# Kernel optimization log

Hardware: AMD Instinct MI355X
Metric: run time of the kernel (lower is better)

Reference implementation:

```python
import jax, jax.numpy as jnp
import numpy as np

B, N = 262144, 64
CLIP_RATIO = 0.2
DUAL_CLIP = 5.0
USE_VALUE_CLIP = True
HALF_LOG_2PI = 0.5 * float(np.log(2.0 * np.pi))


def setup_inputs() -> dict:
    key = jax.random.key(0)
    ks = jax.random.split(key, 9)
    return {
        "mu_new": jax.random.normal(ks[0], (B, N), jnp.float32),
        "sigma_new": jax.random.uniform(ks[1], (B, N), jnp.float32, 0.5, 1.5),
        "mu_old": jax.random.normal(ks[2], (B, N), jnp.float32),
        "sigma_old": jax.random.uniform(ks[3], (B, N), jnp.float32, 0.5, 1.5),
        "action": jax.random.normal(ks[4], (B, N), jnp.float32),
        "value_new": jax.random.normal(ks[5], (B,), jnp.float32),
        "value_old": jax.random.normal(ks[6], (B,), jnp.float32),
        "adv": jax.random.normal(ks[7], (B,), jnp.float32),
        "return_": jax.random.normal(ks[8], (B,), jnp.float32),
        "weight": jnp.ones((B,), jnp.float32),
    }


def _gauss_logprob(action, mu, sigma):
    # independent Normal log-prob, summed over action dim -> (B,)
    z = (action - mu) / sigma
    return jnp.sum(-0.5 * z * z - jnp.log(sigma) - HALF_LOG_2PI, axis=-1)


def reference(mu_new, sigma_new, mu_old, sigma_old, action,
              value_new, value_old, adv, return_, weight):
    logp_new = _gauss_logprob(action, mu_new, sigma_new)   # (B,)
    logp_old = _gauss_logprob(action, mu_old, sigma_old)   # (B,) constant w.r.t. new params
    ratio = jnp.exp(logp_new - logp_old)

    surr1 = ratio * adv
    surr2 = jnp.clip(ratio, 1.0 - CLIP_RATIO, 1.0 + CLIP_RATIO) * adv
    clipped = jnp.minimum(surr1, surr2)
    # dual clip (arXiv:1912.09729 Eq. 5)
    clipped = jnp.maximum(clipped, DUAL_CLIP * adv)
    policy_loss = -jnp.mean(clipped * weight)

    # entropy of diagonal Gaussian, summed over N
    entropy = jnp.sum(0.5 + HALF_LOG_2PI + jnp.log(sigma_new), axis=-1)
    entropy_loss = jnp.mean(entropy * weight)

    if USE_VALUE_CLIP:
        value_clip = value_old + jnp.clip(value_new - value_old, -CLIP_RATIO, CLIP_RATIO)
        v1 = jnp.square(return_ - value_new)
        v2 = jnp.square(return_ - value_clip)
        value_loss = 0.5 * jnp.mean(jnp.maximum(v1, v2) * weight)
    else:
        value_loss = 0.5 * jnp.mean(jnp.square(return_ - value_new) * weight)

    approx_kl = jnp.mean(logp_old - logp_new)
    clipfrac = jnp.mean((jnp.abs(ratio - 1.0) > CLIP_RATIO).astype(jnp.float32))
    return policy_loss, value_loss, entropy_loss, approx_kl, clipfrac
```

## Files before the change

kernel.cpp:

```cpp
#include <hip/hip_runtime.h>

static constexpr int   N_DIM        = 64;
static constexpr float HALF_LOG_2PI = 0.9189385332046727f;
static constexpr float CLIP_RATIO   = 0.2f;
static constexpr float DUAL_CLIP    = 5.0f;
static constexpr int   GRID         = 2048;
static constexpr float ENT_CONST    = (float)N_DIM * (0.5f + HALF_LOG_2PI);
static constexpr float ENT_C16      = ENT_CONST / 16.0f;

__device__ __forceinline__ void ppo_set(const float4& mn, const float4& sn,
                                        const float4& mo, const float4& so,
                                        const float4& a,
                                        float& en_out, float& d_out)
{
    float qn = 0.f, qo = 0.f;
    float pn = 1.f, po = 1.f;
#define PPO_COMP(c) {                                        \
        float rn = __builtin_amdgcn_rcpf(sn.c);              \
        float zn = (a.c - mn.c) * rn;  qn += zn * zn;        \
        float ro = __builtin_amdgcn_rcpf(so.c);              \
        float zo = (a.c - mo.c) * ro;  qo += zo * zo;        \
        pn *= sn.c;  po *= so.c; }
    PPO_COMP(x) PPO_COMP(y) PPO_COMP(z) PPO_COMP(w)
#undef PPO_COMP
    const float en = __logf(pn);
    const float eo = __logf(po);
    en_out = en;
    d_out  = 0.5f * (qo - qn) + (eo - en);
}

__device__ __forceinline__ void ppo_tail(float en, float d, float w, float ad,
                                         float& accP, float& accE,
                                         float& accK, float& accC)
{
    accK -= d;
    accE += w * (en + ENT_C16);
#pragma unroll
    for (int m = 1; m < 16; m <<= 1) d += __shfl_xor(d, m, 16);
    const float ratio = __expf(d);
    const float rc = fminf(fmaxf(ratio, 1.f - CLIP_RATIO), 1.f + CLIP_RATIO);
    float cl = fminf(ratio * ad, rc * ad);
    cl = fmaxf(cl, DUAL_CLIP * ad);
    accP += cl * w;
    accC += (fabsf(ratio - 1.f) > CLIP_RATIO) ? 1.f : 0.f;
}

__global__ __launch_bounds__(256, 4) void ppo_main(
    const float* __restrict__ mu_new,
    const float* __restrict__ sg_new,
    const float* __restrict__ mu_old,
    const float* __restrict__ sg_old,
    const float* __restrict__ act,
    const float* __restrict__ vnew,
    const float* __restrict__ vold,
    const float* __restrict__ adv,
    const float* __restrict__ ret,
    const float* __restrict__ wgt,
    float* __restrict__ ws,
    int b_rows)
{
    const int t    = threadIdx.x;
    const int wave = t >> 6;
    const int lane = t & 63;
    const int sub  = lane >> 4;

    float accP = 0.f, accV = 0.f, accE = 0.f, accK = 0.f, accC = 0.f;

    {
        const int r = blockIdx.x * 256 + t;
        if (r < b_rows) {
            const float vn = vnew[r], vo = vold[r], rt = ret[r], w = wgt[r];
            const float vc = vo + fminf(fmaxf(vn - vo, -CLIP_RATIO), CLIP_RATIO);
            const float d1 = rt - vn, d2 = rt - vc;
            accV += fmaxf(d1 * d1, d2 * d2) * w;
        }
    }

    const int n_sets = b_rows >> 2;
    const int stride = gridDim.x << 2;
    const int lofs   = lane * 4;
    int s = (blockIdx.x << 2) + wave;

#define PPO_LOAD(P) {                                            \
        const int off = (s << 8) + lofs;                         \
        const int r   = (s << 2) + sub;                          \
        P##mn = *(const float4*)(mu_new + off);                  \
        P##sn = *(const float4*)(sg_new + off);                  \
        P##mo = *(const float4*)(mu_old + off);                  \
        P##so = *(const float4*)(sg_old + off);                  \
        P##a  = *(const float4*)(act    + off);                  \
        P##w  = wgt[r];  P##ad = adv[r];                         \
        s += stride; }

#define PPO_COMPUTE(P) {                                         \
        float en, d;                                             \
        ppo_set(P##mn, P##sn, P##mo, P##so, P##a, en, d);        \
        ppo_tail(en, d, P##w, P##ad, accP, accE, accK, accC); }

    if (s < n_sets) {
        float4 Amn, Asn, Amo, Aso, Aa;  float Aw, Aad;
        float4 Bmn, Bsn, Bmo, Bso, Ba;  float Bw, Bad;

        PPO_LOAD(A);
        bool pendA = true;
        while (s < n_sets) {
            PPO_LOAD(B);
            PPO_COMPUTE(A);
            pendA = false;
            if (s < n_sets) { PPO_LOAD(A); pendA = true; }
            PPO_COMPUTE(B);
        }
        if (pendA) PPO_COMPUTE(A);
    }
#undef PPO_LOAD
#undef PPO_COMPUTE

    accP *= 0.0625f;
    accC *= 0.0625f;

#pragma unroll
    for (int m = 1; m < 64; m <<= 1) {
        accP += __shfl_xor(accP, m, 64);
        accV += __shfl_xor(accV, m, 64);
        accE += __shfl_xor(accE, m, 64);
        accK += __shfl_xor(accK, m, 64);
        accC += __shfl_xor(accC, m, 64);
    }

    __shared__ float red[4][5];
    if (lane == 0) {
        red[wave][0] = accP; red[wave][1] = accV; red[wave][2] = accE;
        red[wave][3] = accK; red[wave][4] = accC;
    }
    __syncthreads();

    if (t == 0) {
        float sm[5] = {0.f, 0.f, 0.f, 0.f, 0.f};
#pragma unroll
        for (int wv = 0; wv < 4; ++wv)
#pragma unroll
            for (int k = 0; k < 5; ++k) sm[k] += red[wv][k];
#pragma unroll
        for (int k = 0; k < 5; ++k) ws[k * GRID + blockIdx.x] = sm[k];
    }
}

__global__ __launch_bounds__(320) void ppo_reduce(
    const float* __restrict__ ws, float* __restrict__ out, int b_rows)
{
    const int wave = threadIdx.x >> 6;
    const int lane = threadIdx.x & 63;

    float v = 0.f;
    for (int i = lane; i < GRID; i += 64) v += ws[wave * GRID + i];
#pragma unroll
    for (int m = 1; m < 64; m <<= 1) v += __shfl_xor(v, m, 64);

    if (lane == 0) {
        const float invB = 1.0f / (float)b_rows;
        float o;
        if      (wave == 0) o = -v * invB;
        else if (wave == 1) o = 0.5f * v * invB;
        else                o = v * invB;
        out[wave] = o;
    }
}

extern "C" void kernel_launch(void* const* d_in, const int* in_sizes, int n_in,
                              void* d_out, int out_size, void* d_ws, size_t ws_size,
                              hipStream_t stream) {
    const float* mu_new = (const float*)d_in[0];
    const float* sg_new = (const float*)d_in[1];
    const float* mu_old = (const float*)d_in[2];
    const float* sg_old = (const float*)d_in[3];
    const float* act    = (const float*)d_in[4];
    const float* vnew   = (const float*)d_in[5];
    const float* vold   = (const float*)d_in[6];
    const float* adv    = (const float*)d_in[7];
    const float* ret    = (const float*)d_in[8];
    const float* wgt    = (const float*)d_in[9];
    float* out = (float*)d_out;
    float* ws  = (float*)d_ws;

    const int b_rows = in_sizes[5];

    ppo_main<<<GRID, 256, 0, stream>>>(mu_new, sg_new, mu_old, sg_old, act,
                                       vnew, vold, adv, ret, wgt,
                                       ws, b_rows);
    ppo_reduce<<<1, 320, 0, stream>>>(ws, out, b_rows);
}
```

Measured before the change: 316.0 us.

## Stream row tiles into double-buffered LDS via async global_load_lds

Replaces the direct float4 register loads of the five (B,64) input streams with asynchronous global-to-LDS copies (global_load_lds, 16 bytes per lane) into a per-wave double-buffered shared-memory tile. Explicit s_waitcnt vmcnt waits gate each compute step, and the block reduction scratch is moved into a corner of the same LDS buffer. The aim is to cut vector register pressure from prefetched data and keep more loads in flight on this bandwidth-bound kernel. In exchange it uses about 40KB of LDS per block, which may limit occupancy, and adds LDS read traffic plus hand-managed wait counts.

```diff
diff --git a/kernel.cpp b/kernel.cpp
--- a/kernel.cpp
+++ b/kernel.cpp
@@ -7,6 +7,14 @@
 static constexpr int   GRID         = 2048;
 static constexpr float ENT_CONST    = (float)N_DIM * (0.5f + HALF_LOG_2PI);
 static constexpr float ENT_C16      = ENT_CONST / 16.0f;
+
+__device__ __forceinline__ void async_cp16(const float* g, float* l)
+{
+    __builtin_amdgcn_global_load_lds(
+        (const __attribute__((address_space(1))) void*)g,
+        (__attribute__((address_space(3))) void*)l,
+        16, 0, 0);
+}
 
 __device__ __forceinline__ void ppo_set(const float4& mn, const float4& sn,
                                         const float4& mo, const float4& so,
@@ -59,6 +67,8 @@
     float* __restrict__ ws,
     int b_rows)
 {
+    __shared__ __align__(16) float lds[4][2][5][256];
+
     const int t    = threadIdx.x;
     const int wave = t >> 6;
     const int lane = t & 63;
@@ -78,41 +88,57 @@
 
     const int n_sets = b_rows >> 2;
     const int stride = gridDim.x << 2;
-    const int lofs   = lane * 4;
+    const int lofs   = lane << 2;
     int s = (blockIdx.x << 2) + wave;
 
-#define PPO_LOAD(P) {                                            \
-        const int off = (s << 8) + lofs;                         \
+#define PPO_ISSUE(BUF, P) {                                      \
         const int r   = (s << 2) + sub;                          \
-        P##mn = *(const float4*)(mu_new + off);                  \
-        P##sn = *(const float4*)(sg_new + off);                  \
-        P##mo = *(const float4*)(mu_old + off);                  \
-        P##so = *(const float4*)(sg_old + off);                  \
-        P##a  = *(const float4*)(act    + off);                  \
         P##w  = wgt[r];  P##ad = adv[r];                         \
+        float* lp = &lds[wave][BUF][0][0];                       \
+        const int gof = (s << 8) + lofs;                         \
+        async_cp16(mu_new + gof, lp + 0 * 256);                  \
+        async_cp16(sg_new + gof, lp + 1 * 256);                  \
+        async_cp16(mu_old + gof, lp + 2 * 256);                  \
+        async_cp16(sg_old + gof, lp + 3 * 256);                  \
+        async_cp16(act    + gof, lp + 4 * 256);                  \
         s += stride; }
 
-#define PPO_COMPUTE(P) {                                         \
+#define PPO_WAIT(N) do {                                          \
+        asm volatile("s_waitcnt vmcnt(" #N ")" ::: "memory");     \
+        __builtin_amdgcn_sched_barrier(0); } while (0)
+
+#define PPO_COMPUTE(BUF, P) {                                    \
+        const float* lp = &lds[wave][BUF][0][0];                 \
+        const float4 mn = *(const float4*)(lp + 0 * 256 + lofs); \
+        const float4 sn = *(const float4*)(lp + 1 * 256 + lofs); \
+        const float4 mo = *(const float4*)(lp + 2 * 256 + lofs); \
+        const float4 so = *(const float4*)(lp + 3 * 256 + lofs); \
+        const float4 a  = *(const float4*)(lp + 4 * 256 + lofs); \
         float en, d;                                             \
-        ppo_set(P##mn, P##sn, P##mo, P##so, P##a, en, d);        \
+        ppo_set(mn, sn, mo, so, a, en, d);                       \
         ppo_tail(en, d, P##w, P##ad, accP, accE, accK, accC); }
 
     if (s < n_sets) {
-        float4 Amn, Asn, Amo, Aso, Aa;  float Aw, Aad;
-        float4 Bmn, Bsn, Bmo, Bso, Ba;  float Bw, Bad;
-
-        PPO_LOAD(A);
+        float Aw, Aad, Bw, Bad;
+        PPO_ISSUE(0, A);
         bool pendA = true;
         while (s < n_sets) {
-            PPO_LOAD(B);
-            PPO_COMPUTE(A);
+            PPO_ISSUE(1, B);
+            PPO_WAIT(7);
+            PPO_COMPUTE(0, A);
             pendA = false;
-            if (s < n_sets) { PPO_LOAD(A); pendA = true; }
-            PPO_COMPUTE(B);
+            if (s < n_sets) {
+                PPO_ISSUE(0, A);  pendA = true;
+                PPO_WAIT(7);
+            } else {
+                PPO_WAIT(0);
+            }
+            PPO_COMPUTE(1, B);
         }
-        if (pendA) PPO_COMPUTE(A);
-    }
-#undef PPO_LOAD
+        if (pendA) { PPO_WAIT(0); PPO_COMPUTE(0, A); }
+    }
+#undef PPO_ISSUE
+#undef PPO_WAIT
 #undef PPO_COMPUTE
 
     accP *= 0.0625f;
@@ -127,10 +153,12 @@
         accC += __shfl_xor(accC, m, 64);
     }
 
-    __shared__ float red[4][5];
+    __syncthreads();
+    float* redp = &lds[3][1][4][236];
     if (lane == 0) {
-        red[wave][0] = accP; red[wave][1] = accV; red[wave][2] = accE;
-        red[wave][3] = accK; red[wave][4] = accC;
+        redp[wave * 5 + 0] = accP; redp[wave * 5 + 1] = accV;
+        redp[wave * 5 + 2] = accE; redp[wave * 5 + 3] = accK;
+        redp[wave * 5 + 4] = accC;
     }
     __syncthreads();
 
@@ -139,7 +167,7 @@
 #pragma unroll
         for (int wv = 0; wv < 4; ++wv)
 #pragma unroll
-            for (int k = 0; k < 5; ++k) sm[k] += red[wv][k];
+            for (int k = 0; k < 5; ++k) sm[k] += redp[wv * 5 + k];
 #pragma unroll
         for (int k = 0; k < 5; ++k) ws[k * GRID + blockIdx.x] = sm[k];
     }
```

New measurement: 315.4 us. No clear change (-0.2%).
